# Kernel tuning notes

Hardware: AMD Instinct MI355X
Metric: run time of the kernel (lower is better)

The kernel has to match this reference:

```python
import jax, jax.numpy as jnp
import numpy as np

BN_EPS = 1e-6


def _conv1x1(x, w, b):
    # x: (B, Cin, N, K), w: (Cout, Cin), b: (Cout,)
    return jnp.einsum('oc,bcnk->bonk', w, x) + b[None, :, None, None]


def _bn(x, gamma, beta, mean, var):
    # inference-mode BatchNorm2d over channel axis 1
    inv = gamma / jnp.sqrt(var + BN_EPS)
    return x * inv[None, :, None, None] + (beta - mean * inv)[None, :, None, None]


def setup_inputs() -> dict:
    key = jax.random.key(0)
    ks = jax.random.split(key, 12)
    B, N, K = 4, 16384, 16
    C_out = 32
    C_img = 2 * C_out - 10          # 54, so concat has 2*C_out = 64 channels
    C_in1 = 2 * C_out               # 64
    C_in2 = 2 * (C_out + 3)         # 70

    points = jax.random.normal(ks[0], (B, N, 3), jnp.float32)
    image_features = jax.random.normal(ks[1], (B, C_img, N, K), jnp.float32)
    dist = jax.random.uniform(ks[2], (B, N, K), jnp.float32)
    idx = jax.random.randint(ks[3], (B, N, K), 0, N, dtype=jnp.int32)

    w1 = jax.random.normal(ks[4], (C_out, C_in1), jnp.float32) / np.sqrt(C_in1).astype(np.float32)
    b1 = jnp.zeros((C_out,), jnp.float32)
    gamma1 = jnp.ones((C_out,), jnp.float32)
    beta1 = jnp.zeros((C_out,), jnp.float32)
    mean1 = 0.1 * jax.random.normal(ks[5], (C_out,), jnp.float32)
    var1 = 0.5 + jax.random.uniform(ks[6], (C_out,), jnp.float32)

    w2 = jax.random.normal(ks[7], (C_out, C_in2), jnp.float32) / np.sqrt(C_in2).astype(np.float32)
    b2 = jnp.zeros((C_out,), jnp.float32)
    gamma2 = jnp.ones((C_out,), jnp.float32)
    beta2 = jnp.zeros((C_out,), jnp.float32)
    mean2 = 0.1 * jax.random.normal(ks[8], (C_out,), jnp.float32)
    var2 = 0.5 + jax.random.uniform(ks[9], (C_out,), jnp.float32)

    return {
        'points': points, 'image_features': image_features, 'dist': dist, 'idx': idx,
        'w1': w1, 'b1': b1, 'gamma1': gamma1, 'beta1': beta1, 'mean1': mean1, 'var1': var1,
        'w2': w2, 'b2': b2, 'gamma2': gamma2, 'beta2': beta2, 'mean2': mean2, 'var2': var2,
    }


def reference(points, image_features, dist, idx,
              w1, b1, gamma1, beta1, mean1, var1,
              w2, b2, gamma2, beta2, mean2, var2):
    B, N, K = idx.shape
    pts = jnp.swapaxes(points, 1, 2)                       # (B, 3, N)
    ep = jnp.broadcast_to(pts[:, :, :, None], (B, 3, N, K))  # extended points
    # KNN gather: nb[b, c, n, k] = pts[b, c, idx[b, n, k]]
    nb = jax.vmap(lambda p, i: p[:, i])(pts, idx)          # (B, 3, N, K)

    concat = jnp.concatenate(
        [ep, nb, ep - nb, dist[:, None, :, :], image_features], axis=1)  # (B, 64, N, K)

    h = jax.nn.relu(_bn(_conv1x1(concat, w1, b1), gamma1, beta1, mean1, var1))  # (B, 32, N, K)
    feat = jnp.concatenate([h, ep], axis=1)                # (B, 35, N, K)

    pooled = jnp.concatenate(
        [jnp.max(feat, axis=-1, keepdims=True),
         jnp.mean(feat, axis=-1, keepdims=True)], axis=1)  # (B, 70, N, 1)

    out = jax.nn.relu(_bn(_conv1x1(pooled, w2, b2), gamma2, beta2, mean2, var2))  # (B, 32, N, 1)
    return out
```

## Files before the change

### kernel.cpp

```cpp
#include <hip/hip_runtime.h>
#include <hip/hip_bf16.h>
#include <cmath>

#define BN_EPS 1e-6f
typedef unsigned int u32;
typedef __attribute__((ext_vector_type(8))) short short8;
typedef __attribute__((ext_vector_type(4))) float f32x4;

constexpr int B_    = 4;
constexpr int N_    = 16384;
constexpr int K_    = 16;
constexpr int C_IMG = 54;
constexpr int C1    = 64;
constexpr int CO    = 32;
constexpr int C2    = 70;
constexpr int NT    = 16;
constexpr int POS   = 256;
constexpr int XSTR  = 34;
constexpr int PPAD  = 76;
constexpr int PBSTR = 50;
constexpr int NK    = N_ * K_;

__device__ inline u32 pkbf(float a, float b) {
    union { __hip_bfloat162 h; u32 u; } cv;
    cv.h = __float22bfloat162_rn(make_float2(a, b));
    return cv.u;
}
__device__ inline float bf2f(unsigned short s) {
    union { u32 u; float f; } cv; cv.u = ((u32)s) << 16; return cv.f;
}
__device__ inline int SW(int pos) { return ((pos >> 4) & 7) << 2; }

__global__ __launch_bounds__(256, 4) void pif_mfma_kernel(
    const float* __restrict__ points, const float* __restrict__ imgf,
    const float* __restrict__ dist,   const int*   __restrict__ idx,
    const float* __restrict__ w1, const float* __restrict__ b1,
    const float* __restrict__ g1, const float* __restrict__ be1,
    const float* __restrict__ m1, const float* __restrict__ v1,
    const float* __restrict__ w2, const float* __restrict__ b2,
    const float* __restrict__ g2, const float* __restrict__ be2,
    const float* __restrict__ m2, const float* __restrict__ v2,
    float* __restrict__ out)
{
    __shared__ u32   x_lds[POS * XSTR];
    __shared__ float pooled[NT][PPAD];

    const int t   = threadIdx.x;
    const int tpb = N_ / NT;
    const int b   = blockIdx.x / tpb;
    const int n0  = (blockIdx.x % tpb) * NT;
    const int k   = t & 15, ln = t >> 4, n = n0 + ln;
    const int w = t >> 6, lane = t & 63, m16 = lane & 15, quad = lane >> 4;

    const int   base_nk = (b * N_ + n) * K_ + k;
    const int   j  = idx[base_nk];
    const float dv = dist[base_nk];
    const int   pb = (b * N_ + n) * 3;
    const float px = points[pb], py = points[pb + 1], pz = points[pb + 2];
    const int   qb = (b * N_ + j) * 3;
    const float qx = points[qb], qy = points[qb + 1], qz = points[qb + 2];

    {
        u32* row = &x_lds[t * XSTR];
        const int s = SW(t);
        row[0 ^ s] = pkbf(px, py);
        row[1 ^ s] = pkbf(pz, qx);
        row[2 ^ s] = pkbf(qy, qz);
        row[3 ^ s] = pkbf(px - qx, py - qy);
        row[4 ^ s] = pkbf(pz - qz, dv);
    }

    {
        const int nn = (t >> 2) & 15, q = t & 3;
        const int swn = ((nn & 7) << 2);
        const float* bbase = imgf + (size_t)b * C_IMG * NK + (n0 + nn) * K_ + 4 * q;
        #pragma unroll
        for (int it = 0; it < 7; ++it) {
            const int pp = w + 4 * it;
            if (pp < 27) {
                const float4 L0 = *(const float4*)(bbase + (size_t)(2 * pp)     * NK);
                const float4 L1 = *(const float4*)(bbase + (size_t)(2 * pp + 1) * NK);
                const int col = (5 + pp) ^ swn;
                u32* r0 = &x_lds[(nn * 16 + 4 * q) * XSTR + col];
                r0[0 * XSTR] = pkbf(L0.x, L1.x);
                r0[1 * XSTR] = pkbf(L0.y, L1.y);
                r0[2 * XSTR] = pkbf(L0.z, L1.z);
                r0[3 * XSTR] = pkbf(L0.w, L1.w);
            }
        }
    }

    short8 bfrag[2][2];
    float  inv1v[2], add1v[2];
    #pragma unroll
    for (int ot = 0; ot < 2; ++ot) {
        const int o = ot * 16 + m16;
        #pragma unroll
        for (int kc = 0; kc < 2; ++kc) {
            const float* wr = w1 + o * C1 + kc * 32 + quad * 8;
            union { u32 u[4]; short8 v; } bf;
            bf.u[0] = pkbf(wr[0], wr[1]); bf.u[1] = pkbf(wr[2], wr[3]);
            bf.u[2] = pkbf(wr[4], wr[5]); bf.u[3] = pkbf(wr[6], wr[7]);
            bfrag[ot][kc] = bf.v;
        }
        const float iv = g1[o] * rsqrtf(v1[o] + BN_EPS);
        inv1v[ot] = iv;
        add1v[ot] = be1[o] - m1[o] * iv + b1[o] * iv;
    }

    short8 w2frag[3];
    float  add2 = 0.f;
    if (w < 2) {
        const int o = w * 16 + m16;
        const float iv2 = g2[o] * rsqrtf(v2[o] + BN_EPS);
        add2 = be2[o] - m2[o] * iv2 + b2[o] * iv2;
        #pragma unroll
        for (int kc = 0; kc < 3; ++kc) {
            float wv[8];
            #pragma unroll
            for (int jj = 0; jj < 8; ++jj) {
                const int c = kc * 32 + quad * 8 + jj;
                wv[jj] = (c < C2) ? iv2 * w2[o * C2 + c] : 0.f;
            }
            union { u32 u[4]; short8 v; } bf;
            bf.u[0] = pkbf(wv[0], wv[1]); bf.u[1] = pkbf(wv[2], wv[3]);
            bf.u[2] = pkbf(wv[4], wv[5]); bf.u[3] = pkbf(wv[6], wv[7]);
            w2frag[kc] = bf.v;
        }
    }

    if (t < 48) {
        const int nn = t & 15, jj = t >> 4;
        const float v = points[(b * N_ + n0 + nn) * 3 + jj];
        pooled[nn][32 + jj] = v;
        pooled[nn][67 + jj] = v;
    }

    __syncthreads();

    f32x4 acc[4][2];
    #pragma unroll
    for (int mt = 0; mt < 4; ++mt)
        #pragma unroll
        for (int ot = 0; ot < 2; ++ot)
            acc[mt][ot] = (f32x4){0.f, 0.f, 0.f, 0.f};

    #pragma unroll
    for (int mt = 0; mt < 4; ++mt) {
        const int posr = w * 64 + mt * 16 + m16;
        const int s    = ((w * 4 + mt) & 7) << 2;
        #pragma unroll
        for (int kc = 0; kc < 2; ++kc) {
            const int colb = (kc * 16 + quad * 4) ^ s;
            const u32* r2 = &x_lds[posr * XSTR + colb];
            uint2 a0 = *(const uint2*)r2;
            uint2 a1 = *(const uint2*)(r2 + 2);
            union { u32 u[4]; short8 v; } af;
            af.u[0] = a0.x; af.u[1] = a0.y; af.u[2] = a1.x; af.u[3] = a1.y;
            acc[mt][0] = __builtin_amdgcn_mfma_f32_16x16x32_bf16(af.v, bfrag[0][kc], acc[mt][0], 0, 0, 0);
            acc[mt][1] = __builtin_amdgcn_mfma_f32_16x16x32_bf16(af.v, bfrag[1][kc], acc[mt][1], 0, 0, 0);
        }
    }

    #pragma unroll
    for (int mt = 0; mt < 4; ++mt) {
        #pragma unroll
        for (int ot = 0; ot < 2; ++ot) {
            float mx = 0.f, sm = 0.f;
            #pragma unroll
            for (int r = 0; r < 4; ++r) {
                float hv = fmaf(acc[mt][ot][r], inv1v[ot], add1v[ot]);
                hv = fmaxf(hv, 0.f);
                mx = fmaxf(mx, hv);
                sm += hv;
            }
            mx = fmaxf(mx, __shfl_xor(mx, 16));
            mx = fmaxf(mx, __shfl_xor(mx, 32));
            sm += __shfl_xor(sm, 16);
            sm += __shfl_xor(sm, 32);
            if (quad == 0) {
                const int nn = w * 4 + mt;
                pooled[nn][ot * 16 + m16]      = mx;
                pooled[nn][35 + ot * 16 + m16] = sm * (1.f / 16.f);
            }
        }
    }
    __syncthreads();

    u32* pbf_hi = &x_lds[0];
    u32* pbf_lo = &x_lds[NT * PBSTR];
    {
        const int nn = t >> 4, j0 = t & 15;
        #pragma unroll
        for (int r = 0; r < 3; ++r) {
            const int jj = j0 + 16 * r;
            const int c0 = 2 * jj, c1 = 2 * jj + 1;
            const float v0 = (c0 < C2) ? pooled[nn][c0] : 0.f;
            const float v1_ = (c1 < C2) ? pooled[nn][c1] : 0.f;
            const u32 hi = pkbf(v0, v1_);
            const float r0 = v0 - bf2f((unsigned short)(hi & 0xffff));
            const float r1 = v1_ - bf2f((unsigned short)(hi >> 16));
            pbf_hi[nn * PBSTR + jj] = hi;
            pbf_lo[nn * PBSTR + jj] = pkbf(r0, r1);
        }
    }
    __syncthreads();

    if (w < 2) {
        f32x4 d = (f32x4){0.f, 0.f, 0.f, 0.f};
        #pragma unroll
        for (int half = 0; half < 2; ++half) {
            const u32* pb_ = half ? pbf_lo : pbf_hi;
            #pragma unroll
            for (int kc = 0; kc < 3; ++kc) {
                const u32* r2 = &pb_[m16 * PBSTR + kc * 16 + quad * 4];
                uint2 a0 = *(const uint2*)r2;
                uint2 a1 = *(const uint2*)(r2 + 2);
                union { u32 u[4]; short8 v; } af;
                af.u[0] = a0.x; af.u[1] = a0.y; af.u[2] = a1.x; af.u[3] = a1.y;
                d = __builtin_amdgcn_mfma_f32_16x16x32_bf16(af.v, w2frag[kc], d, 0, 0, 0);
            }
        }
        const int o = w * 16 + m16;
        f32x4 ov;
        #pragma unroll
        for (int r = 0; r < 4; ++r) ov[r] = fmaxf(d[r] + add2, 0.f);
        float4* dst = (float4*)&out[(size_t)(b * CO + o) * N_ + n0 + quad * 4];
        *dst = make_float4(ov[0], ov[1], ov[2], ov[3]);
    }
}

extern "C" void kernel_launch(void* const* d_in, const int* in_sizes, int n_in,
                              void* d_out, int out_size, void* d_ws, size_t ws_size,
                              hipStream_t stream) {
    const float* points = (const float*)d_in[0];
    const float* imgf   = (const float*)d_in[1];
    const float* dist   = (const float*)d_in[2];
    const int*   idx    = (const int*)  d_in[3];
    const float* w1     = (const float*)d_in[4];
    const float* b1     = (const float*)d_in[5];
    const float* g1     = (const float*)d_in[6];
    const float* be1    = (const float*)d_in[7];
    const float* m1     = (const float*)d_in[8];
    const float* v1     = (const float*)d_in[9];
    const float* w2     = (const float*)d_in[10];
    const float* b2     = (const float*)d_in[11];
    const float* g2     = (const float*)d_in[12];
    const float* be2    = (const float*)d_in[13];
    const float* m2     = (const float*)d_in[14];
    const float* v2     = (const float*)d_in[15];
    float* out          = (float*)d_out;

    const int blocks = B_ * (N_ / NT);
    pif_mfma_kernel<<<blocks, 256, 0, stream>>>(
        points, imgf, dist, idx,
        w1, b1, g1, be1, m1, v1,
        w2, b2, g2, be2, m2, v2, out);
}
```

Baseline: 356.9 us.

## Transpose activation LDS tile to channel-major layout and issue image loads first

Stores the staged bf16 activations channel-pair-major (32 rows of 260 positions) instead of position-major with XOR swizzle. Image-feature writes become single 128-bit LDS stores and the MFMA A-fragment reads become four scalar loads across rows. The image-feature global loads are moved ahead of the idx and points gathers to expose memory latency earlier, and the w1 fragment loads are vectorised to float4. This trades wider LDS stores for more, narrower LDS reads in the MFMA loop.

After: 360.5 us. About the same (+1.0%).

```diff
diff --git a/kernel.cpp b/kernel.cpp
--- a/kernel.cpp
+++ b/kernel.cpp
@@ -16,7 +16,7 @@
 constexpr int C2    = 70;
 constexpr int NT    = 16;
 constexpr int POS   = 256;
-constexpr int XSTR  = 34;
+constexpr int PSTR  = 260;
 constexpr int PPAD  = 76;
 constexpr int PBSTR = 50;
 constexpr int NK    = N_ * K_;
@@ -29,7 +29,6 @@
 __device__ inline float bf2f(unsigned short s) {
     union { u32 u; float f; } cv; cv.u = ((u32)s) << 16; return cv.f;
 }
-__device__ inline int SW(int pos) { return ((pos >> 4) & 7) << 2; }
 
 __global__ __launch_bounds__(256, 4) void pif_mfma_kernel(
     const float* __restrict__ points, const float* __restrict__ imgf,
@@ -42,7 +41,7 @@
     const float* __restrict__ m2, const float* __restrict__ v2,
     float* __restrict__ out)
 {
-    __shared__ u32   x_lds[POS * XSTR];
+    __shared__ u32   x_lds[32 * PSTR];
     __shared__ float pooled[NT][PPAD];
 
     const int t   = threadIdx.x;
@@ -51,6 +50,25 @@
     const int n0  = (blockIdx.x % tpb) * NT;
     const int k   = t & 15, ln = t >> 4, n = n0 + ln;
     const int w = t >> 6, lane = t & 63, m16 = lane & 15, quad = lane >> 4;
+
+    {
+        const int nn = (t >> 2) & 15, q = t & 3;
+        const int laneoff = (n0 + nn) * K_ + 4 * q;
+        const float* ibase = imgf + (size_t)b * C_IMG * NK + laneoff;
+        const int pps0 = __builtin_amdgcn_readfirstlane(w);
+        #pragma unroll
+        for (int it = 0; it < 7; ++it) {
+            const int pp = pps0 + 4 * it;
+            if (pp < 27) {
+                const float* p0 = ibase + (size_t)(2 * pp) * NK;
+                const float4 L0 = *(const float4*)p0;
+                const float4 L1 = *(const float4*)(p0 + NK);
+                *(uint4*)&x_lds[(5 + pp) * PSTR + nn * 16 + 4 * q] =
+                    make_uint4(pkbf(L0.x, L1.x), pkbf(L0.y, L1.y),
+                               pkbf(L0.z, L1.z), pkbf(L0.w, L1.w));
+            }
+        }
+    }
 
     const int   base_nk = (b * N_ + n) * K_ + k;
     const int   j  = idx[base_nk];
@@ -60,35 +78,11 @@
     const int   qb = (b * N_ + j) * 3;
     const float qx = points[qb], qy = points[qb + 1], qz = points[qb + 2];
 
-    {
-        u32* row = &x_lds[t * XSTR];
-        const int s = SW(t);
-        row[0 ^ s] = pkbf(px, py);
-        row[1 ^ s] = pkbf(pz, qx);
-        row[2 ^ s] = pkbf(qy, qz);
-        row[3 ^ s] = pkbf(px - qx, py - qy);
-        row[4 ^ s] = pkbf(pz - qz, dv);
-    }
-
-    {
-        const int nn = (t >> 2) & 15, q = t & 3;
-        const int swn = ((nn & 7) << 2);
-        const float* bbase = imgf + (size_t)b * C_IMG * NK + (n0 + nn) * K_ + 4 * q;
-        #pragma unroll
-        for (int it = 0; it < 7; ++it) {
-            const int pp = w + 4 * it;
-            if (pp < 27) {
-                const float4 L0 = *(const float4*)(bbase + (size_t)(2 * pp)     * NK);
-                const float4 L1 = *(const float4*)(bbase + (size_t)(2 * pp + 1) * NK);
-                const int col = (5 + pp) ^ swn;
-                u32* r0 = &x_lds[(nn * 16 + 4 * q) * XSTR + col];
-                r0[0 * XSTR] = pkbf(L0.x, L1.x);
-                r0[1 * XSTR] = pkbf(L0.y, L1.y);
-                r0[2 * XSTR] = pkbf(L0.z, L1.z);
-                r0[3 * XSTR] = pkbf(L0.w, L1.w);
-            }
-        }
-    }
+    x_lds[0 * PSTR + t] = pkbf(px, py);
+    x_lds[1 * PSTR + t] = pkbf(pz, qx);
+    x_lds[2 * PSTR + t] = pkbf(qy, qz);
+    x_lds[3 * PSTR + t] = pkbf(px - qx, py - qy);
+    x_lds[4 * PSTR + t] = pkbf(pz - qz, dv);
 
     short8 bfrag[2][2];
     float  inv1v[2], add1v[2];
@@ -98,9 +92,11 @@
         #pragma unroll
         for (int kc = 0; kc < 2; ++kc) {
             const float* wr = w1 + o * C1 + kc * 32 + quad * 8;
+            const float4 W0 = *(const float4*)wr;
+            const float4 W1 = *(const float4*)(wr + 4);
             union { u32 u[4]; short8 v; } bf;
-            bf.u[0] = pkbf(wr[0], wr[1]); bf.u[1] = pkbf(wr[2], wr[3]);
-            bf.u[2] = pkbf(wr[4], wr[5]); bf.u[3] = pkbf(wr[6], wr[7]);
+            bf.u[0] = pkbf(W0.x, W0.y); bf.u[1] = pkbf(W0.z, W0.w);
+            bf.u[2] = pkbf(W1.x, W1.y); bf.u[3] = pkbf(W1.z, W1.w);
             bfrag[ot][kc] = bf.v;
         }
         const float iv = g1[o] * rsqrtf(v1[o] + BN_EPS);
@@ -147,16 +143,13 @@
 
     #pragma unroll
     for (int mt = 0; mt < 4; ++mt) {
-        const int posr = w * 64 + mt * 16 + m16;
-        const int s    = ((w * 4 + mt) & 7) << 2;
+        const int pos = w * 64 + mt * 16 + m16;
         #pragma unroll
         for (int kc = 0; kc < 2; ++kc) {
-            const int colb = (kc * 16 + quad * 4) ^ s;
-            const u32* r2 = &x_lds[posr * XSTR + colb];
-            uint2 a0 = *(const uint2*)r2;
-            uint2 a1 = *(const uint2*)(r2 + 2);
             union { u32 u[4]; short8 v; } af;
-            af.u[0] = a0.x; af.u[1] = a0.y; af.u[2] = a1.x; af.u[3] = a1.y;
+            #pragma unroll
+            for (int c = 0; c < 4; ++c)
+                af.u[c] = x_lds[(kc * 16 + quad * 4 + c) * PSTR + pos];
             acc[mt][0] = __builtin_amdgcn_mfma_f32_16x16x32_bf16(af.v, bfrag[0][kc], acc[mt][0], 0, 0, 0);
             acc[mt][1] = __builtin_amdgcn_mfma_f32_16x16x32_bf16(af.v, bfrag[1][kc], acc[mt][1], 0, 0, 0);
         }
@@ -195,10 +188,10 @@
         for (int r = 0; r < 3; ++r) {
             const int jj = j0 + 16 * r;
             const int c0 = 2 * jj, c1 = 2 * jj + 1;
-            const float v0 = (c0 < C2) ? pooled[nn][c0] : 0.f;
+            const float v0  = (c0 < C2) ? pooled[nn][c0] : 0.f;
             const float v1_ = (c1 < C2) ? pooled[nn][c1] : 0.f;
             const u32 hi = pkbf(v0, v1_);
-            const float r0 = v0 - bf2f((unsigned short)(hi & 0xffff));
+            const float r0 = v0  - bf2f((unsigned short)(hi & 0xffff));
             const float r1 = v1_ - bf2f((unsigned short)(hi >> 16));
             pbf_hi[nn * PBSTR + jj] = hi;
             pbf_lo[nn * PBSTR + jj] = pkbf(r0, r1);
```
